# Performance work log

Measured on AMD Instinct MI355X. Metric: run time of the kernel, lower is better.

Reference implementation:

```python
import jax, jax.numpy as jnp
import numpy as np

N = 100000      # nodes
E = 640000      # total edges across all relations
D_IN = 128
D_OUT = 128
R = 8           # num_rel
B = 4           # num_bases


def setup_inputs() -> dict:
    key = jax.random.key(0)
    ks = jax.random.split(key, 7)
    return {
        "X": jax.random.normal(ks[0], (N, D_IN), dtype=jnp.float32),
        "edge_src": jax.random.randint(ks[1], (E,), 0, N, dtype=jnp.int32),
        "edge_dst": jax.random.randint(ks[2], (E,), 0, N, dtype=jnp.int32),
        "edge_rel": jax.random.randint(ks[3], (E,), 0, R, dtype=jnp.int32),
        "edge_val": jax.random.uniform(ks[4], (E,), dtype=jnp.float32),
        "w_bases": jax.random.normal(ks[5], (B, D_IN, D_OUT), dtype=jnp.float32) * 0.05,
        "w_rel": jax.random.normal(ks[6], (R, B), dtype=jnp.float32) * 0.5,
    }


def reference(X, edge_src, edge_dst, edge_rel, edge_val, w_bases, w_rel):
    # Per-relation SpMM: support_r = A_r @ X, where A_r rows are destinations.
    # Fuse all relations into one gather + one segmented scatter-add.
    msg = X[edge_src] * edge_val[:, None]                      # [E, D_IN]
    seg = edge_rel.astype(jnp.int32) * N + edge_dst            # combined (rel, dst) id
    supports = jax.ops.segment_sum(msg, seg, num_segments=R * N)
    supports = supports.reshape(R, N, D_IN)                    # == concat of per-rel supports
    # Basis-decomposed relation weights: w[r] = sum_b w_rel[r,b] * w_bases[b]
    w = jnp.einsum("rb,bio->rio", w_rel, w_bases)              # [R, D_IN, D_OUT]
    # cat(supports, dim=1) @ w.view(R*D_IN, D_OUT) == sum_r supports_r @ w_r
    out = jnp.einsum("rni,rio->no", supports, w)               # [N, D_OUT]
    return out
```

## Files before the change

kernel.cpp:

```cpp
#include <hip/hip_runtime.h>
#include <stdint.h>

#define D_IN 128
#define D_OUT 128
#define NREL 8
#define NBASE 4

typedef __attribute__((ext_vector_type(8))) short short8;
typedef __attribute__((ext_vector_type(4))) float floatx4;
typedef __attribute__((ext_vector_type(2))) float floatx2;

__device__ __forceinline__ unsigned short f2bf(float f) {
  unsigned int u = __float_as_uint(f);
  u += 0x7fffu + ((u >> 16) & 1u);
  return (unsigned short)(u >> 16);
}
__device__ __forceinline__ unsigned pack2bf(float lo, float hi) {
  return (unsigned)f2bf(lo) | ((unsigned)f2bf(hi) << 16);
}
__device__ __forceinline__ float bflo(unsigned int u) { return __uint_as_float(u << 16); }
__device__ __forceinline__ float bfhi(unsigned int u) { return __uint_as_float(u & 0xffff0000u); }

__global__ void k_prep(const float4* __restrict__ X, ushort4* __restrict__ Xb, int n4,
                       const float* __restrict__ w_bases, unsigned short* __restrict__ W2T,
                       uint4* __restrict__ counts4, int nc4) {
  int i = blockIdx.x * blockDim.x + threadIdx.x;
  if (i < n4) {
    float4 v = X[i];
    ushort4 o;
    o.x = f2bf(v.x); o.y = f2bf(v.y); o.z = f2bf(v.z); o.w = f2bf(v.w);
    Xb[i] = o;
  }
  if (i < 128 * 512) {
    int o = i >> 9, c = i & 511;
    int k = c >> 2, b = c & 3;
    W2T[i] = f2bf(w_bases[(b * D_IN + k) * D_OUT + o]);
  }
  if (i < nc4) counts4[i] = make_uint4(0u, 0u, 0u, 0u);
}

__global__ void k_count(const int* __restrict__ dst, int* __restrict__ counts, int E) {
  int i = blockIdx.x * blockDim.x + threadIdx.x;
  if (i < E) atomicAdd(&counts[dst[i]], 1);
}

__global__ void k_scan1(const int* __restrict__ counts, int* __restrict__ localsc,
                        int* __restrict__ bsum, int Nn) {
  __shared__ int s[256];
  int i = blockIdx.x * 256 + threadIdx.x;
  int v = (i < Nn) ? counts[i] : 0;
  s[threadIdx.x] = v;
  __syncthreads();
  for (int off = 1; off < 256; off <<= 1) {
    int t = 0;
    if (threadIdx.x >= off) t = s[threadIdx.x - off];
    __syncthreads();
    s[threadIdx.x] += t;
    __syncthreads();
  }
  if (i < Nn) localsc[i] = s[threadIdx.x] - v;
  if (threadIdx.x == 255) bsum[blockIdx.x] = s[255];
}

__global__ void k_scan23(const int* __restrict__ localsc, const int* __restrict__ bsum,
                         int* __restrict__ offsets, int* __restrict__ cursor, int Nn, int E) {
  __shared__ int red[256];
  int acc = 0;
  for (int j = threadIdx.x; j < blockIdx.x; j += 256) acc += bsum[j];
  red[threadIdx.x] = acc;
  __syncthreads();
  for (int off = 128; off > 0; off >>= 1) {
    if (threadIdx.x < off) red[threadIdx.x] += red[threadIdx.x + off];
    __syncthreads();
  }
  int pref = red[0];
  int i = blockIdx.x * 256 + threadIdx.x;
  if (i < Nn) {
    int v = localsc[i] + pref;
    offsets[i] = v;
    cursor[i] = v;
  }
  if (i == 0) offsets[Nn] = E;
}

__global__ void k_bucket(const int* __restrict__ src, const int* __restrict__ dst,
                         const int* __restrict__ rel, const float* __restrict__ val,
                         const float* __restrict__ w_rel, int* __restrict__ cursor,
                         unsigned* __restrict__ srcs, float4* __restrict__ coef, int E) {
  int i = blockIdx.x * blockDim.x + threadIdx.x;
  if (i >= E) return;
  int d = dst[i];
  int pos = atomicAdd(&cursor[d], 1);
  float v = val[i];
  const float4 w = *(const float4*)(w_rel + rel[i] * 4);
  srcs[pos] = (unsigned)src[i];
  coef[pos] = make_float4(v * w.x, v * w.y, v * w.z, v * w.w);
}

__global__ __launch_bounds__(256)
void k_agg_gemm(const unsigned* __restrict__ esrc, const float4* __restrict__ ecoef,
                const int* __restrict__ offsets, const unsigned* __restrict__ Xb2,
                const unsigned short* __restrict__ W2T, float* __restrict__ out, int Nn) {
  __shared__ __align__(16) unsigned short aggS[32][520];

  const int wave = threadIdx.x >> 6, lane = threadIdx.x & 63;
  const int d0 = blockIdx.x * 32 + wave * 8;
  const floatx2 zf2 = {0.f, 0.f};

  int oidx = d0 + (lane < 8 ? lane : 8);
  if (oidx > Nn) oidx = Nn;
  const int offv = offsets[oidx];
  const int s0 = __shfl(offv, 0);
  const int e8 = __shfl(offv, 8);

  floatx2 a0 = zf2, a1 = zf2, a2 = zf2, a3 = zf2;
  int row = 0;
  int bnd = __shfl(offv, 1);

#define FLUSH()                                                      \
  do {                                                               \
    uint4 o_;                                                        \
    o_.x = pack2bf(a0.x, a1.x);                                      \
    o_.y = pack2bf(a2.x, a3.x);                                      \
    o_.z = pack2bf(a0.y, a1.y);                                      \
    o_.w = pack2bf(a2.y, a3.y);                                      \
    *(uint4*)&aggS[wave * 8 + row][lane * 8] = o_;                   \
    a0 = zf2; a1 = zf2; a2 = zf2; a3 = zf2;                          \
    ++row;                                                           \
    bnd = (row < 8) ? __shfl(offv, row + 1) : 0x7fffffff;            \
  } while (0)

#define ACCT(EI, Y, C)                                               \
  do {                                                               \
    if ((EI) < e8) {                                                 \
      while ((EI) == bnd) FLUSH();                                   \
      floatx2 x_;                                                    \
      x_.x = bflo(Y);                                                \
      x_.y = bfhi(Y);                                                \
      a0 += (C).x * x_;                                              \
      a1 += (C).y * x_;                                              \
      a2 += (C).z * x_;                                              \
      a3 += (C).w * x_;                                              \
    }                                                                \
  } while (0)

#define LOADG(P, BASE)                                               \
  do {                                                               \
    int e0_ = (BASE);                                                \
    int e1_ = e0_ + 1; if (e1_ > ce) e1_ = ce;                       \
    int e2_ = e0_ + 2; if (e2_ > ce) e2_ = ce;                       \
    int e3_ = e0_ + 3; if (e3_ > ce) e3_ = ce;                       \
    s##P##0 = esrc[e0_]; s##P##1 = esrc[e1_];                        \
    s##P##2 = esrc[e2_]; s##P##3 = esrc[e3_];                        \
    y##P##0 = Xb2[((size_t)s##P##0 << 6) + lane];                    \
    y##P##1 = Xb2[((size_t)s##P##1 << 6) + lane];                    \
    y##P##2 = Xb2[((size_t)s##P##2 << 6) + lane];                    \
    y##P##3 = Xb2[((size_t)s##P##3 << 6) + lane];                    \
    c##P##0 = ecoef[e0_]; c##P##1 = ecoef[e1_];                      \
    c##P##2 = ecoef[e2_]; c##P##3 = ecoef[e3_];                      \
  } while (0)

  if (s0 < e8) {
    const int ce = e8 - 1;
    unsigned sA0, sA1, sA2, sA3, yA0, yA1, yA2, yA3;
    unsigned sB0, sB1, sB2, sB3, yB0, yB1, yB2, yB3;
    float4 cA0, cA1, cA2, cA3, cB0, cB1, cB2, cB3;
    LOADG(A, s0);
    int gi = s0;
    int par = 0;
    while (gi < e8) {
      const int gn = gi + 4;
      if (par == 0) {
        if (gn < e8) LOADG(B, gn);
        ACCT(gi, yA0, cA0);
        ACCT(gi + 1, yA1, cA1);
        ACCT(gi + 2, yA2, cA2);
        ACCT(gi + 3, yA3, cA3);
      } else {
        if (gn < e8) LOADG(A, gn);
        ACCT(gi, yB0, cB0);
        ACCT(gi + 1, yB1, cB1);
        ACCT(gi + 2, yB2, cB2);
        ACCT(gi + 3, yB3, cB3);
      }
      par ^= 1;
      gi = gn;
    }
  }
  while (row < 8) FLUSH();

  __syncthreads();

  const int q = lane >> 4, r16 = lane & 15;
  const int wn = wave * 32;
  const floatx4 zero = {0.f, 0.f, 0.f, 0.f};
  floatx4 acc[2][2];
  acc[0][0] = zero; acc[0][1] = zero; acc[1][0] = zero; acc[1][1] = zero;

#pragma unroll 4
  for (int k0 = 0; k0 < 512; k0 += 32) {
    int ka = k0 + q * 8;
    short8 af[2], bfv[2];
    af[0] = *(const short8*)&aggS[r16][ka];
    af[1] = *(const short8*)&aggS[16 + r16][ka];
    bfv[0] = *(const short8*)(W2T + (size_t)(wn + r16) * 512 + ka);
    bfv[1] = *(const short8*)(W2T + (size_t)(wn + 16 + r16) * 512 + ka);
#pragma unroll
    for (int i = 0; i < 2; ++i)
#pragma unroll
      for (int j = 0; j < 2; ++j)
        acc[i][j] = __builtin_amdgcn_mfma_f32_16x16x32_bf16(af[i], bfv[j], acc[i][j], 0, 0, 0);
  }

#pragma unroll
  for (int i = 0; i < 2; ++i) {
#pragma unroll
    for (int j = 0; j < 2; ++j) {
#pragma unroll
      for (int p = 0; p < 4; ++p) {
        int prow = i * 16 + q * 4 + p;
        int col = wn + j * 16 + r16;
        int grow = blockIdx.x * 32 + prow;
        if (grow < Nn) out[(size_t)grow * 128 + col] = acc[i][j][p];
      }
    }
  }
}

extern "C" void kernel_launch(void* const* d_in, const int* in_sizes, int n_in,
                              void* d_out, int out_size, void* d_ws, size_t ws_size,
                              hipStream_t stream) {
  const float* X = (const float*)d_in[0];
  const int* esrc = (const int*)d_in[1];
  const int* edst = (const int*)d_in[2];
  const int* erel = (const int*)d_in[3];
  const float* eval_ = (const float*)d_in[4];
  const float* w_bases = (const float*)d_in[5];
  const float* w_rel = (const float*)d_in[6];
  const int Nn = in_sizes[0] / D_IN;
  const int E = in_sizes[1];

  char* ws = (char*)d_ws;
  size_t off = 0;
  auto alloc = [&](size_t bytes) -> char* {
    char* p = ws + off;
    off += (bytes + 255) & ~(size_t)255;
    return p;
  };
  unsigned short* Xb = (unsigned short*)alloc((size_t)Nn * D_IN * 2);
  unsigned short* W2T = (unsigned short*)alloc((size_t)128 * 512 * 2);
  int* counts = (int*)alloc((size_t)Nn * 4);
  int* cursor = (int*)alloc((size_t)Nn * 4);
  int* offsets = (int*)alloc((size_t)(Nn + 1) * 4);
  int* localsc = (int*)alloc((size_t)Nn * 4);
  int* bsum = (int*)alloc(4096);
  unsigned* srcs = (unsigned*)alloc((size_t)E * 4);
  float4* coef = (float4*)alloc((size_t)E * 16);
  (void)ws_size;

  int n4 = Nn * D_IN / 4;
  int nc4 = Nn / 4;
  k_prep<<<(n4 + 255) / 256, 256, 0, stream>>>((const float4*)X, (ushort4*)Xb, n4,
                                               w_bases, W2T, (uint4*)counts, nc4);

  k_count<<<(E + 255) / 256, 256, 0, stream>>>(edst, counts, E);
  int nb = (Nn + 255) / 256;
  k_scan1<<<nb, 256, 0, stream>>>(counts, localsc, bsum, Nn);
  k_scan23<<<nb, 256, 0, stream>>>(localsc, bsum, offsets, cursor, Nn, E);
  k_bucket<<<(E + 255) / 256, 256, 0, stream>>>(esrc, edst, erel, eval_, w_rel,
                                                cursor, srcs, coef, E);

  k_agg_gemm<<<(Nn + 31) / 32, 256, 0, stream>>>(srcs, coef, offsets,
                                                 (const unsigned*)Xb, W2T,
                                                 (float*)d_out, Nn);
}
```

Measured before the change: 290.2 us.

## Pack edge src/rel/val into uint2 and load edge chunks cooperatively via shuffles

The bucketing kernel now writes one 8-byte record per edge (source index with the relation id in its high bits, plus the raw edge value) instead of a 4-byte source and a 16-byte float4 coefficient. The aggregation kernel rebuilds the four coefficients from a shared-memory copy of w_rel. It also loads edge records in 64-edge chunks, one per lane, and broadcasts them with shuffles, where before every lane loaded each edge redundantly. This cuts edge-array traffic and scalar loads, at the cost of extra shuffles and multiplies in the inner loop.

```diff
diff --git a/kernel.cpp b/kernel.cpp
--- a/kernel.cpp
+++ b/kernel.cpp
@@ -85,23 +85,22 @@
 
 __global__ void k_bucket(const int* __restrict__ src, const int* __restrict__ dst,
                          const int* __restrict__ rel, const float* __restrict__ val,
-                         const float* __restrict__ w_rel, int* __restrict__ cursor,
-                         unsigned* __restrict__ srcs, float4* __restrict__ coef, int E) {
+                         int* __restrict__ cursor, uint2* __restrict__ bucket, int E) {
   int i = blockIdx.x * blockDim.x + threadIdx.x;
   if (i >= E) return;
   int d = dst[i];
   int pos = atomicAdd(&cursor[d], 1);
-  float v = val[i];
-  const float4 w = *(const float4*)(w_rel + rel[i] * 4);
-  srcs[pos] = (unsigned)src[i];
-  coef[pos] = make_float4(v * w.x, v * w.y, v * w.z, v * w.w);
+  bucket[pos] = make_uint2((unsigned)src[i] | ((unsigned)rel[i] << 21), __float_as_uint(val[i]));
 }
 
 __global__ __launch_bounds__(256)
-void k_agg_gemm(const unsigned* __restrict__ esrc, const float4* __restrict__ ecoef,
-                const int* __restrict__ offsets, const unsigned* __restrict__ Xb2,
+void k_agg_gemm(const uint2* __restrict__ bucket, const int* __restrict__ offsets,
+                const float* __restrict__ w_rel_g, const unsigned* __restrict__ Xb2,
                 const unsigned short* __restrict__ W2T, float* __restrict__ out, int Nn) {
   __shared__ __align__(16) unsigned short aggS[32][520];
+  __shared__ __align__(16) float wrS[NREL * NBASE];
+  if (threadIdx.x < NREL * NBASE) wrS[threadIdx.x] = w_rel_g[threadIdx.x];
+  __syncthreads();
 
   const int wave = threadIdx.x >> 6, lane = threadIdx.x & 63;
   const int d0 = blockIdx.x * 32 + wave * 8;
@@ -130,41 +129,63 @@
     bnd = (row < 8) ? __shfl(offv, row + 1) : 0x7fffffff;            \
   } while (0)
 
-#define ACCT(EI, Y, C)                                               \
+#define ACCT(EI, R, V, Y)                                            \
   do {                                                               \
     if ((EI) < e8) {                                                 \
       while ((EI) == bnd) FLUSH();                                   \
+      const float4 w_ = *(const float4*)&wrS[((R) >> 21) * 4];       \
+      const float val_ = __uint_as_float(V);                         \
+      const float c0_ = val_ * w_.x, c1_ = val_ * w_.y;              \
+      const float c2_ = val_ * w_.z, c3_ = val_ * w_.w;              \
       floatx2 x_;                                                    \
       x_.x = bflo(Y);                                                \
       x_.y = bfhi(Y);                                                \
-      a0 += (C).x * x_;                                              \
-      a1 += (C).y * x_;                                              \
-      a2 += (C).z * x_;                                              \
-      a3 += (C).w * x_;                                              \
+      a0 += c0_ * x_;                                                \
+      a1 += c1_ * x_;                                                \
+      a2 += c2_ * x_;                                                \
+      a3 += c3_ * x_;                                                \
     }                                                                \
   } while (0)
 
 #define LOADG(P, BASE)                                               \
   do {                                                               \
-    int e0_ = (BASE);                                                \
-    int e1_ = e0_ + 1; if (e1_ > ce) e1_ = ce;                       \
-    int e2_ = e0_ + 2; if (e2_ > ce) e2_ = ce;                       \
-    int e3_ = e0_ + 3; if (e3_ > ce) e3_ = ce;                       \
-    s##P##0 = esrc[e0_]; s##P##1 = esrc[e1_];                        \
-    s##P##2 = esrc[e2_]; s##P##3 = esrc[e3_];                        \
-    y##P##0 = Xb2[((size_t)s##P##0 << 6) + lane];                    \
-    y##P##1 = Xb2[((size_t)s##P##1 << 6) + lane];                    \
-    y##P##2 = Xb2[((size_t)s##P##2 << 6) + lane];                    \
-    y##P##3 = Xb2[((size_t)s##P##3 << 6) + lane];                    \
-    c##P##0 = ecoef[e0_]; c##P##1 = ecoef[e1_];                      \
-    c##P##2 = ecoef[e2_]; c##P##3 = ecoef[e3_];                      \
+    const int gb_ = (BASE);                                          \
+    if (gb_ - cbase >= 64) {                                         \
+      cbase += 64;                                                   \
+      chC = chN;                                                     \
+      int in_ = cbase + 64 + lane;                                   \
+      if (in_ > ce) in_ = ce;                                        \
+      chN = bucket[in_];                                             \
+    }                                                                \
+    const int j0_ = gb_ - cbase;                                     \
+    int t1_ = gb_ + 1; if (t1_ > ce) t1_ = ce;                       \
+    int t2_ = gb_ + 2; if (t2_ > ce) t2_ = ce;                       \
+    int t3_ = gb_ + 3; if (t3_ > ce) t3_ = ce;                       \
+    const int j1_ = t1_ - cbase, j2_ = t2_ - cbase, j3_ = t3_ - cbase; \
+    r##P##0 = __shfl(chC.x, j0_); v##P##0 = __shfl(chC.y, j0_);      \
+    r##P##1 = __shfl(chC.x, j1_); v##P##1 = __shfl(chC.y, j1_);      \
+    r##P##2 = __shfl(chC.x, j2_); v##P##2 = __shfl(chC.y, j2_);      \
+    r##P##3 = __shfl(chC.x, j3_); v##P##3 = __shfl(chC.y, j3_);      \
+    y##P##0 = Xb2[((size_t)(r##P##0 & 0x1FFFFFu) << 6) + lane];      \
+    y##P##1 = Xb2[((size_t)(r##P##1 & 0x1FFFFFu) << 6) + lane];      \
+    y##P##2 = Xb2[((size_t)(r##P##2 & 0x1FFFFFu) << 6) + lane];      \
+    y##P##3 = Xb2[((size_t)(r##P##3 & 0x1FFFFFu) << 6) + lane];      \
   } while (0)
 
   if (s0 < e8) {
     const int ce = e8 - 1;
-    unsigned sA0, sA1, sA2, sA3, yA0, yA1, yA2, yA3;
-    unsigned sB0, sB1, sB2, sB3, yB0, yB1, yB2, yB3;
-    float4 cA0, cA1, cA2, cA3, cB0, cB1, cB2, cB3;
+    int cbase = s0;
+    uint2 chC, chN;
+    {
+      int i0 = cbase + lane;
+      if (i0 > ce) i0 = ce;
+      chC = bucket[i0];
+      int i1 = cbase + 64 + lane;
+      if (i1 > ce) i1 = ce;
+      chN = bucket[i1];
+    }
+    unsigned rA0, rA1, rA2, rA3, vA0, vA1, vA2, vA3, yA0, yA1, yA2, yA3;
+    unsigned rB0, rB1, rB2, rB3, vB0, vB1, vB2, vB3, yB0, yB1, yB2, yB3;
     LOADG(A, s0);
     int gi = s0;
     int par = 0;
@@ -172,16 +193,16 @@
       const int gn = gi + 4;
       if (par == 0) {
         if (gn < e8) LOADG(B, gn);
-        ACCT(gi, yA0, cA0);
-        ACCT(gi + 1, yA1, cA1);
-        ACCT(gi + 2, yA2, cA2);
-        ACCT(gi + 3, yA3, cA3);
+        ACCT(gi, rA0, vA0, yA0);
+        ACCT(gi + 1, rA1, vA1, yA1);
+        ACCT(gi + 2, rA2, vA2, yA2);
+        ACCT(gi + 3, rA3, vA3, yA3);
       } else {
         if (gn < e8) LOADG(A, gn);
-        ACCT(gi, yB0, cB0);
-        ACCT(gi + 1, yB1, cB1);
-        ACCT(gi + 2, yB2, cB2);
-        ACCT(gi + 3, yB3, cB3);
+        ACCT(gi, rB0, vB0, yB0);
+        ACCT(gi + 1, rB1, vB1, yB1);
+        ACCT(gi + 2, rB2, vB2, yB2);
+        ACCT(gi + 3, rB3, vB3, yB3);
       }
       par ^= 1;
       gi = gn;
@@ -254,8 +275,7 @@
   int* offsets = (int*)alloc((size_t)(Nn + 1) * 4);
   int* localsc = (int*)alloc((size_t)Nn * 4);
   int* bsum = (int*)alloc(4096);
-  unsigned* srcs = (unsigned*)alloc((size_t)E * 4);
-  float4* coef = (float4*)alloc((size_t)E * 16);
+  uint2* bucket = (uint2*)alloc((size_t)E * 8);
   (void)ws_size;
 
   int n4 = Nn * D_IN / 4;
@@ -267,10 +287,9 @@
   int nb = (Nn + 255) / 256;
   k_scan1<<<nb, 256, 0, stream>>>(counts, localsc, bsum, Nn);
   k_scan23<<<nb, 256, 0, stream>>>(localsc, bsum, offsets, cursor, Nn, E);
-  k_bucket<<<(E + 255) / 256, 256, 0, stream>>>(esrc, edst, erel, eval_, w_rel,
-                                                cursor, srcs, coef, E);
-
-  k_agg_gemm<<<(Nn + 31) / 32, 256, 0, stream>>>(srcs, coef, offsets,
+  k_bucket<<<(E + 255) / 256, 256, 0, stream>>>(esrc, edst, erel, eval_, cursor, bucket, E);
+
+  k_agg_gemm<<<(Nn + 31) / 32, 256, 0, stream>>>(bucket, offsets, w_rel,
                                                  (const unsigned*)Xb, W2T,
                                                  (float*)d_out, Nn);
 }
```

After: 264.0 us. 1.1x faster.

## Deepen gather prefetch pipeline in aggregation and fold edge counting into prep

Applied to the files above, without the earlier changes.

The aggregation loop moves from double-buffered loads of 4 edges to a six-slot rotating pipeline. Source indices are fetched four groups ahead, X rows are gathered three groups ahead and coefficients one group ahead, so more gather latency can be hidden. The separate count kernel is merged into the prep kernel, with a memset zeroing the counts, and cross-lane broadcasts of offsets use readlane instead of shfl. The kernel also gets a 4-blocks-per-CU occupancy hint, which together with the many live prefetch registers risks spills or reduced occupancy.

```diff
diff --git a/kernel.cpp b/kernel.cpp
--- a/kernel.cpp
+++ b/kernel.cpp
@@ -23,7 +23,7 @@
 
 __global__ void k_prep(const float4* __restrict__ X, ushort4* __restrict__ Xb, int n4,
                        const float* __restrict__ w_bases, unsigned short* __restrict__ W2T,
-                       uint4* __restrict__ counts4, int nc4) {
+                       const int* __restrict__ edst, int* __restrict__ counts, int E) {
   int i = blockIdx.x * blockDim.x + threadIdx.x;
   if (i < n4) {
     float4 v = X[i];
@@ -36,12 +36,7 @@
     int k = c >> 2, b = c & 3;
     W2T[i] = f2bf(w_bases[(b * D_IN + k) * D_OUT + o]);
   }
-  if (i < nc4) counts4[i] = make_uint4(0u, 0u, 0u, 0u);
-}
-
-__global__ void k_count(const int* __restrict__ dst, int* __restrict__ counts, int E) {
-  int i = blockIdx.x * blockDim.x + threadIdx.x;
-  if (i < E) atomicAdd(&counts[dst[i]], 1);
+  if (i < E) atomicAdd(&counts[edst[i]], 1);
 }
 
 __global__ void k_scan1(const int* __restrict__ counts, int* __restrict__ localsc,
@@ -97,8 +92,8 @@
   coef[pos] = make_float4(v * w.x, v * w.y, v * w.z, v * w.w);
 }
 
-__global__ __launch_bounds__(256)
-void k_agg_gemm(const unsigned* __restrict__ esrc, const float4* __restrict__ ecoef,
+__global__ __launch_bounds__(256, 4)
+void k_agg_gemm(const unsigned* __restrict__ esrcs, const float4* __restrict__ ecoef,
                 const int* __restrict__ offsets, const unsigned* __restrict__ Xb2,
                 const unsigned short* __restrict__ W2T, float* __restrict__ out, int Nn) {
   __shared__ __align__(16) unsigned short aggS[32][520];
@@ -110,12 +105,12 @@
   int oidx = d0 + (lane < 8 ? lane : 8);
   if (oidx > Nn) oidx = Nn;
   const int offv = offsets[oidx];
-  const int s0 = __shfl(offv, 0);
-  const int e8 = __shfl(offv, 8);
+  const int s0 = __builtin_amdgcn_readlane(offv, 0);
+  const int e8 = __builtin_amdgcn_readlane(offv, 8);
 
   floatx2 a0 = zf2, a1 = zf2, a2 = zf2, a3 = zf2;
   int row = 0;
-  int bnd = __shfl(offv, 1);
+  int bnd = __builtin_amdgcn_readlane(offv, 1);
 
 #define FLUSH()                                                      \
   do {                                                               \
@@ -127,10 +122,41 @@
     *(uint4*)&aggS[wave * 8 + row][lane * 8] = o_;                   \
     a0 = zf2; a1 = zf2; a2 = zf2; a3 = zf2;                          \
     ++row;                                                           \
-    bnd = (row < 8) ? __shfl(offv, row + 1) : 0x7fffffff;            \
-  } while (0)
-
-#define ACCT(EI, Y, C)                                               \
+    bnd = (row < 8) ? __builtin_amdgcn_readlane(offv, row + 1)       \
+                    : 0x7fffffff;                                    \
+  } while (0)
+
+#define SSRC(S, BASE)                                                \
+  do {                                                               \
+    int b_ = (BASE);                                                 \
+    int t0_ = b_ < ce ? b_ : ce;                                     \
+    int t1_ = b_ + 1 < ce ? b_ + 1 : ce;                             \
+    int t2_ = b_ + 2 < ce ? b_ + 2 : ce;                             \
+    int t3_ = b_ + 3 < ce ? b_ + 3 : ce;                             \
+    s##S##0 = esrcs[t0_]; s##S##1 = esrcs[t1_];                      \
+    s##S##2 = esrcs[t2_]; s##S##3 = esrcs[t3_];                      \
+  } while (0)
+
+#define GATH(S)                                                      \
+  do {                                                               \
+    y##S##0 = Xb2[((size_t)s##S##0 << 6) + lane];                    \
+    y##S##1 = Xb2[((size_t)s##S##1 << 6) + lane];                    \
+    y##S##2 = Xb2[((size_t)s##S##2 << 6) + lane];                    \
+    y##S##3 = Xb2[((size_t)s##S##3 << 6) + lane];                    \
+  } while (0)
+
+#define SCOEF(S, BASE)                                               \
+  do {                                                               \
+    int b_ = (BASE);                                                 \
+    int t0_ = b_ < ce ? b_ : ce;                                     \
+    int t1_ = b_ + 1 < ce ? b_ + 1 : ce;                             \
+    int t2_ = b_ + 2 < ce ? b_ + 2 : ce;                             \
+    int t3_ = b_ + 3 < ce ? b_ + 3 : ce;                             \
+    c##S##0 = ecoef[t0_]; c##S##1 = ecoef[t1_];                      \
+    c##S##2 = ecoef[t2_]; c##S##3 = ecoef[t3_];                      \
+  } while (0)
+
+#define ACCT1(EI, C, Y)                                              \
   do {                                                               \
     if ((EI) < e8) {                                                 \
       while ((EI) == bnd) FLUSH();                                   \
@@ -144,47 +170,34 @@
     }                                                                \
   } while (0)
 
-#define LOADG(P, BASE)                                               \
-  do {                                                               \
-    int e0_ = (BASE);                                                \
-    int e1_ = e0_ + 1; if (e1_ > ce) e1_ = ce;                       \
-    int e2_ = e0_ + 2; if (e2_ > ce) e2_ = ce;                       \
-    int e3_ = e0_ + 3; if (e3_ > ce) e3_ = ce;                       \
-    s##P##0 = esrc[e0_]; s##P##1 = esrc[e1_];                        \
-    s##P##2 = esrc[e2_]; s##P##3 = esrc[e3_];                        \
-    y##P##0 = Xb2[((size_t)s##P##0 << 6) + lane];                    \
-    y##P##1 = Xb2[((size_t)s##P##1 << 6) + lane];                    \
-    y##P##2 = Xb2[((size_t)s##P##2 << 6) + lane];                    \
-    y##P##3 = Xb2[((size_t)s##P##3 << 6) + lane];                    \
-    c##P##0 = ecoef[e0_]; c##P##1 = ecoef[e1_];                      \
-    c##P##2 = ecoef[e2_]; c##P##3 = ecoef[e3_];                      \
+#define ACCT4(S, EI0)                                                \
+  do {                                                               \
+    ACCT1((EI0), c##S##0, y##S##0);                                  \
+    ACCT1((EI0) + 1, c##S##1, y##S##1);                              \
+    ACCT1((EI0) + 2, c##S##2, y##S##2);                              \
+    ACCT1((EI0) + 3, c##S##3, y##S##3);                              \
   } while (0)
 
   if (s0 < e8) {
     const int ce = e8 - 1;
-    unsigned sA0, sA1, sA2, sA3, yA0, yA1, yA2, yA3;
-    unsigned sB0, sB1, sB2, sB3, yB0, yB1, yB2, yB3;
-    float4 cA0, cA1, cA2, cA3, cB0, cB1, cB2, cB3;
-    LOADG(A, s0);
+    unsigned s00, s01, s02, s03, s10, s11, s12, s13, s20, s21, s22, s23;
+    unsigned s30, s31, s32, s33, s40, s41, s42, s43, s50, s51, s52, s53;
+    unsigned y00, y01, y02, y03, y10, y11, y12, y13, y20, y21, y22, y23;
+    unsigned y30, y31, y32, y33, y40, y41, y42, y43, y50, y51, y52, y53;
+    float4 c00, c01, c02, c03, c10, c11, c12, c13, c20, c21, c22, c23;
+    float4 c30, c31, c32, c33, c40, c41, c42, c43, c50, c51, c52, c53;
+    SSRC(0, s0); SSRC(1, s0 + 4); SSRC(2, s0 + 8); SSRC(3, s0 + 12);
+    GATH(0); GATH(1); GATH(2);
+    SCOEF(0, s0);
     int gi = s0;
-    int par = 0;
     while (gi < e8) {
-      const int gn = gi + 4;
-      if (par == 0) {
-        if (gn < e8) LOADG(B, gn);
-        ACCT(gi, yA0, cA0);
-        ACCT(gi + 1, yA1, cA1);
-        ACCT(gi + 2, yA2, cA2);
-        ACCT(gi + 3, yA3, cA3);
-      } else {
-        if (gn < e8) LOADG(A, gn);
-        ACCT(gi, yB0, cB0);
-        ACCT(gi + 1, yB1, cB1);
-        ACCT(gi + 2, yB2, cB2);
-        ACCT(gi + 3, yB3, cB3);
-      }
-      par ^= 1;
-      gi = gn;
+      SSRC(4, gi + 16); GATH(3); SCOEF(1, gi + 4); ACCT4(0, gi);
+      SSRC(5, gi + 20); GATH(4); SCOEF(2, gi + 8); ACCT4(1, gi + 4);
+      SSRC(0, gi + 24); GATH(5); SCOEF(3, gi + 12); ACCT4(2, gi + 8);
+      SSRC(1, gi + 28); GATH(0); SCOEF(4, gi + 16); ACCT4(3, gi + 12);
+      SSRC(2, gi + 32); GATH(1); SCOEF(5, gi + 20); ACCT4(4, gi + 16);
+      SSRC(3, gi + 36); GATH(2); SCOEF(0, gi + 24); ACCT4(5, gi + 20);
+      gi += 24;
     }
   }
   while (row < 8) FLUSH();
@@ -259,11 +272,10 @@
   (void)ws_size;
 
   int n4 = Nn * D_IN / 4;
-  int nc4 = Nn / 4;
+  hipMemsetAsync(counts, 0, (size_t)Nn * 4, stream);
   k_prep<<<(n4 + 255) / 256, 256, 0, stream>>>((const float4*)X, (ushort4*)Xb, n4,
-                                               w_bases, W2T, (uint4*)counts, nc4);
-
-  k_count<<<(E + 255) / 256, 256, 0, stream>>>(edst, counts, E);
+                                               w_bases, W2T, edst, counts, E);
+
   int nb = (Nn + 255) / 256;
   k_scan1<<<nb, 256, 0, stream>>>(counts, localsc, bsum, Nn);
   k_scan23<<<nb, 256, 0, stream>>>(localsc, bsum, offsets, cursor, Nn, E);
```

Result: faster. 249.9 us (-13.9%).
